# Optimization experiments

Hardware: AMD Instinct MI355X
Metric: run time of the kernel (lower is better)

Reference implementation:

```python
import jax, jax.numpy as jnp
import numpy as np

D_MODEL = 1024
N_HEADS = 16
N_GROUPS = 4
HEAD_DIM = D_MODEL // N_HEADS          # 64
HPG = N_HEADS // N_GROUPS              # heads per group = 4
KV_DIM = N_GROUPS * HEAD_DIM           # 256


def setup_inputs() -> dict:
    key = jax.random.key(0)
    ks = jax.random.split(key, 9)
    B, T = 2, 2048
    s = 0.02
    return {
        "x":  jax.random.normal(ks[0], (B, T, D_MODEL), dtype=jnp.float32),
        "Wq": jax.random.normal(ks[1], (D_MODEL, D_MODEL), dtype=jnp.float32) * s,
        "bq": jnp.zeros((D_MODEL,), dtype=jnp.float32),
        "Wk": jax.random.normal(ks[2], (D_MODEL, KV_DIM), dtype=jnp.float32) * s,
        "bk": jnp.zeros((KV_DIM,), dtype=jnp.float32),
        "Wv": jax.random.normal(ks[3], (D_MODEL, KV_DIM), dtype=jnp.float32) * s,
        "bv": jnp.zeros((KV_DIM,), dtype=jnp.float32),
        "Wo": jax.random.normal(ks[4], (D_MODEL, D_MODEL), dtype=jnp.float32) * s,
        "bo": jnp.zeros((D_MODEL,), dtype=jnp.float32),
    }


def reference(x, Wq, bq, Wk, bk, Wv, bv, Wo, bo):
    B, T, C = x.shape
    q = x @ Wq + bq                                   # [B,T,C]
    k = x @ Wk + bk                                   # [B,T,G*hd]
    v = x @ Wv + bv

    # [B, G, hpg, T, hd] for q; [B, G, T, hd] for k,v (native GQA head sharing,
    # equivalent to repeat_interleave on the group dim in the torch code)
    q = q.reshape(B, T, N_GROUPS, HPG, HEAD_DIM).transpose(0, 2, 3, 1, 4)
    k = k.reshape(B, T, N_GROUPS, HEAD_DIM).transpose(0, 2, 1, 3)
    v = v.reshape(B, T, N_GROUPS, HEAD_DIM).transpose(0, 2, 1, 3)

    scale = 1.0 / jnp.sqrt(jnp.float32(HEAD_DIM))
    attn = jnp.einsum('bghqd,bgkd->bghqk', q, k) * scale   # [B,G,hpg,T,T]

    causal = jnp.tril(jnp.ones((T, T), dtype=bool))        # True = keep
    attn = jnp.where(causal, attn, jnp.float32(-jnp.inf))
    attn = jax.nn.softmax(attn, axis=-1)
    # dropout p=0.1 only in training mode; reference is eval mode (identity)

    out = jnp.einsum('bghqk,bgkd->bghqd', attn, v)         # [B,G,hpg,T,hd]
    out = out.transpose(0, 3, 1, 2, 4).reshape(B, T, C)
    return out @ Wo + bo
```

## Files before the change

### kernel.cpp

```cpp
#include <hip/hip_runtime.h>
#include <hip/hip_bf16.h>
#include <stdint.h>

#define D_MODEL 1024
#define T_LEN   2048
#define BATCH   2
#define N_HEADS 16
#define KV_DIM  256
#define QKV_N   1536
#define M_ROWS  (BATCH * T_LEN)

typedef unsigned short u16;
typedef __bf16 bf16x8 __attribute__((ext_vector_type(8)));
typedef __bf16 bf16x2 __attribute__((ext_vector_type(2)));
typedef float  f32x4  __attribute__((ext_vector_type(4)));

__device__ __forceinline__ u16 f2b(float f) {
    uint32_t u = __builtin_bit_cast(uint32_t, f);
    u += 0x7FFFu + ((u >> 16) & 1u);
    return (u16)(u >> 16);
}

__device__ __forceinline__ uint32_t pk_bf16(float a, float b) {
#if __has_builtin(__builtin_amdgcn_cvt_pk_bf16_f32)
    bf16x2 v = __builtin_amdgcn_cvt_pk_bf16_f32(a, b);
    return __builtin_bit_cast(uint32_t, v);
#else
    return (uint32_t)f2b(a) | ((uint32_t)f2b(b) << 16);
#endif
}

__device__ __forceinline__ void gl_lds16(const void* g, void* l) {
    __builtin_amdgcn_global_load_lds(g, l, 16, 0, 0);
}

__global__ __launch_bounds__(256) void prep(
    const float* __restrict__ x,
    const float* __restrict__ Wq, const float* __restrict__ Wk,
    const float* __restrict__ Wv, const float* __restrict__ Wo,
    u16* __restrict__ xb, u16* __restrict__ WcatT, u16* __restrict__ WoT)
{
    __shared__ u16 tile[32][33];
    int id = blockIdx.x;
    int tid = threadIdx.x;
    if (id < 2048) {
        int i = (id * 256 + tid) * 8;
        float4 a = *(const float4*)&x[i];
        float4 c = *(const float4*)&x[i + 4];
        u16 r[8] = { f2b(a.x), f2b(a.y), f2b(a.z), f2b(a.w),
                     f2b(c.x), f2b(c.y), f2b(c.z), f2b(c.w) };
        *(uint4*)&xb[i] = *(const uint4*)r;
        return;
    }
    int t = id - 2048;
    int bx = t % 80;
    int k0 = (t / 80) * 32;
    const float* src; u16* dst; int N, n0;
    if (bx < 32)       { src = Wq; dst = WcatT;                   N = 1024; n0 = bx * 32; }
    else if (bx < 40)  { src = Wk; dst = WcatT + 1024 * 1024;     N = 256;  n0 = (bx - 32) * 32; }
    else if (bx < 48)  { src = Wv; dst = WcatT + 1280 * 1024;     N = 256;  n0 = (bx - 40) * 32; }
    else               { src = Wo; dst = WoT;                     N = 1024; n0 = (bx - 48) * 32; }
    for (int i = 0; i < 4; ++i) {
        int idx = tid + i * 256;
        int r = idx >> 5, c = idx & 31;
        tile[r][c] = f2b(src[(size_t)(k0 + r) * N + (n0 + c)]);
    }
    __syncthreads();
    for (int i = 0; i < 4; ++i) {
        int idx = tid + i * 256;
        int r = idx >> 5, c = idx & 31;
        dst[(size_t)(n0 + r) * 1024 + (k0 + c)] = tile[c][r];
    }
}

__global__ __launch_bounds__(256) void gemm_qkv(
    const u16* __restrict__ A, const u16* __restrict__ BT,
    const float* __restrict__ bq, const float* __restrict__ bk,
    const float* __restrict__ bv, u16* __restrict__ Qb,
    u16* __restrict__ Kpack, u16* __restrict__ Vpack)
{
    constexpr int K = 1024;
    constexpr float SCALE = 0.125f * 1.44269504088896f;
    __shared__ __align__(16) u16 As[64 * 64];
    __shared__ __align__(16) u16 Bs[128 * 64];

    int tid  = threadIdx.x;
    int lane = tid & 63, w = tid >> 6;
    int quad = lane >> 4, l15 = lane & 15;
    int m0 = blockIdx.y * 64, n0 = blockIdx.x * 128;
    int lr = lane >> 3, lc = (lane & 7) * 8;

    f32x4 acc[4][2] = {};

    for (int k0 = 0; k0 < K; k0 += 64) {
        for (int t = 0; t < 2; ++t) {
            int rb = t * 32 + w * 8;
            gl_lds16(&A[(size_t)(m0 + rb + lr) * K + k0 + lc], &As[rb * 64]);
        }
        for (int t = 0; t < 4; ++t) {
            int rb = t * 32 + w * 8;
            gl_lds16(&BT[(size_t)(n0 + rb + lr) * K + k0 + lc], &Bs[rb * 64]);
        }
        __syncthreads();
        for (int kk = 0; kk < 64; kk += 32) {
            bf16x8 a[4], b[2];
            for (int i = 0; i < 4; ++i)
                a[i] = *(const bf16x8*)&As[(i * 16 + l15) * 64 + kk + quad * 8];
            for (int j = 0; j < 2; ++j)
                b[j] = *(const bf16x8*)&Bs[(w * 32 + j * 16 + l15) * 64 + kk + quad * 8];
            for (int i = 0; i < 4; ++i)
                for (int j = 0; j < 2; ++j)
                    acc[i][j] = __builtin_amdgcn_mfma_f32_16x16x32_bf16(
                        a[i], b[j], acc[i][j], 0, 0, 0);
        }
        __syncthreads();
    }

    for (int j = 0; j < 2; ++j) {
        int col = n0 + w * 32 + j * 16 + l15;
        float bj = (col < 1024) ? bq[col] : (col < 1280) ? bk[col - 1024] : bv[col - 1280];
        for (int i = 0; i < 4; ++i) {
            int rowb = m0 + i * 16 + quad * 4;
            int bb = rowb >> 11, keyloc = rowb & 2047;
            int t64 = keyloc >> 6;
            if (col < 1024) {
                for (int r = 0; r < 4; ++r)
                    Qb[(size_t)(rowb + r) * 1024 + col] =
                        f2b((acc[i][j][r] + bj) * SCALE);
            } else if (col < 1280) {
                int d = col - 1024; int g = d >> 6; d &= 63;
                int kk = d >> 5, qd = (d >> 3) & 3, e = d & 7;
                int ntk = (keyloc >> 4) & 3, l15k = keyloc & 15;
                size_t base = ((((size_t)(bb * 4 + g) * 32 + t64) * 2 + kk) * 4
                               + ntk) * 512 + qd * 128 + l15k * 8 + e;
                for (int r = 0; r < 4; ++r)
                    Kpack[base + r * 8] = f2b(acc[i][j][r] + bj);
            } else {
                int d = col - 1280; int g = d >> 6; d &= 63;
                int dt = d >> 4, l15v = d & 15;
                int kkp = (keyloc >> 5) & 1, qv = (keyloc >> 3) & 3, e0 = keyloc & 7;
                u16 tmp[4];
                for (int r = 0; r < 4; ++r) tmp[r] = f2b(acc[i][j][r] + bj);
                size_t base = ((((size_t)(bb * 4 + g) * 32 + t64) * 2 + kkp) * 4
                               + dt) * 512 + (qv * 16 + l15v) * 8 + e0;
                *(uint64_t*)&Vpack[base] = *(const uint64_t*)tmp;
            }
        }
    }
}

__global__ __launch_bounds__(256) void gemm_out(
    const u16* __restrict__ A, const u16* __restrict__ BT,
    const float* __restrict__ bias, float* __restrict__ C)
{
    constexpr int K = 1024, N = 1024;
    __shared__ __align__(16) u16 As[64 * 64];
    __shared__ __align__(16) u16 Bs[128 * 64];

    int tid  = threadIdx.x;
    int lane = tid & 63, w = tid >> 6;
    int quad = lane >> 4, l15 = lane & 15;
    int m0 = blockIdx.y * 64, n0 = blockIdx.x * 128;
    int lr = lane >> 3, lc = (lane & 7) * 8;

    f32x4 acc[4][2] = {};

    for (int k0 = 0; k0 < K; k0 += 64) {
        for (int t = 0; t < 2; ++t) {
            int rb = t * 32 + w * 8;
            gl_lds16(&A[(size_t)(m0 + rb + lr) * K + k0 + lc], &As[rb * 64]);
        }
        for (int t = 0; t < 4; ++t) {
            int rb = t * 32 + w * 8;
            gl_lds16(&BT[(size_t)(n0 + rb + lr) * K + k0 + lc], &Bs[rb * 64]);
        }
        __syncthreads();
        for (int kk = 0; kk < 64; kk += 32) {
            bf16x8 a[4], b[2];
            for (int i = 0; i < 4; ++i)
                a[i] = *(const bf16x8*)&As[(i * 16 + l15) * 64 + kk + quad * 8];
            for (int j = 0; j < 2; ++j)
                b[j] = *(const bf16x8*)&Bs[(w * 32 + j * 16 + l15) * 64 + kk + quad * 8];
            for (int i = 0; i < 4; ++i)
                for (int j = 0; j < 2; ++j)
                    acc[i][j] = __builtin_amdgcn_mfma_f32_16x16x32_bf16(
                        a[i], b[j], acc[i][j], 0, 0, 0);
        }
        __syncthreads();
    }

    for (int j = 0; j < 2; ++j) {
        int col = n0 + w * 32 + j * 16 + l15;
        float bj = bias[col];
        for (int i = 0; i < 4; ++i) {
            int rowb = m0 + i * 16 + quad * 4;
            for (int r = 0; r < 4; ++r)
                C[(size_t)(rowb + r) * N + col] = acc[i][j][r] + bj;
        }
    }
}

__global__ __launch_bounds__(64, 4) void attn_kernel(
    const u16* __restrict__ Qb,
    const u16* __restrict__ Kpack,
    const u16* __restrict__ Vpack,
    u16* __restrict__ AO)
{
    constexpr int LDP = 72;
    __shared__ __align__(16) u16 Pw[16 * LDP];

    int lane = threadIdx.x & 63;
    int quad = lane >> 4, l15 = lane & 15;

    int gid = blockIdx.x;
    int b = gid & 1, g = (gid >> 1) & 3;
    int hw = (gid >> 3) & 3;
    int s = gid >> 5;
    int j = 127 - s;
    int head = g * 4 + hw;
    int q0 = j * 16;
    int iters = (j >> 2) + 1;

    const u16* Qp = Qb + ((size_t)b * T_LEN + q0) * 1024 + head * 64;
    const u16* Kp = Kpack + (size_t)(b * 4 + g) * 131072 + (size_t)lane * 8;
    const u16* Vp = Vpack + (size_t)(b * 4 + g) * 131072 + (size_t)lane * 8;
    u16*       Op = AO + ((size_t)b * T_LEN + q0) * D_MODEL + head * 64;

    bf16x8 Qfrag[2];
    #pragma unroll
    for (int kk = 0; kk < 2; ++kk)
        Qfrag[kk] = *(const bf16x8*)&Qp[(size_t)l15 * 1024 + kk * 32 + quad * 8];

    f32x4 o[4] = {};
    float lsum = 0.f;

    for (int tg = 0; tg < iters; ++tg) {
        bool diag = (tg == iters - 1);

        const u16* kb = Kp + (size_t)tg * 4096;
        bf16x8 aK[2][4];
        #pragma unroll
        for (int kk = 0; kk < 2; ++kk)
            #pragma unroll
            for (int ntk = 0; ntk < 4; ++ntk)
                aK[kk][ntk] = *(const bf16x8*)(kb + (kk * 4 + ntk) * 512);

        f32x4 sacc[4] = {};
        #pragma unroll
        for (int kk = 0; kk < 2; ++kk) {
            bf16x8 bQ = Qfrag[kk];
            #pragma unroll
            for (int ntk = 0; ntk < 4; ++ntk)
                sacc[ntk] = __builtin_amdgcn_mfma_f32_16x16x32_bf16(
                    aK[kk][ntk], bQ, sacc[ntk], 0, 0, 0);
        }
        int qrow = q0 + l15;
        float lacc = 0.f;
        #pragma unroll
        for (int ntk = 0; ntk < 4; ++ntk) {
            float p0, p1, p2, p3;
            if (diag) {
                int key = tg * 64 + ntk * 16 + quad * 4;
                p0 = (key + 0 <= qrow) ? exp2f(sacc[ntk][0]) : 0.f;
                p1 = (key + 1 <= qrow) ? exp2f(sacc[ntk][1]) : 0.f;
                p2 = (key + 2 <= qrow) ? exp2f(sacc[ntk][2]) : 0.f;
                p3 = (key + 3 <= qrow) ? exp2f(sacc[ntk][3]) : 0.f;
            } else {
                p0 = exp2f(sacc[ntk][0]);
                p1 = exp2f(sacc[ntk][1]);
                p2 = exp2f(sacc[ntk][2]);
                p3 = exp2f(sacc[ntk][3]);
            }
            lacc += (p0 + p1) + (p2 + p3);
            uint2 pv;
            pv.x = pk_bf16(p0, p1);
            pv.y = pk_bf16(p2, p3);
            *(uint2*)&Pw[l15 * LDP + ntk * 16 + quad * 4] = pv;
        }
        lsum += lacc;

        const u16* vb = Vp + (size_t)tg * 4096;
        #pragma unroll
        for (int kkp = 0; kkp < 2; ++kkp) {
            bf16x8 bV[4];
            #pragma unroll
            for (int dt = 0; dt < 4; ++dt)
                bV[dt] = *(const bf16x8*)(vb + (kkp * 4 + dt) * 512);
            bf16x8 aP = *(const bf16x8*)&Pw[l15 * LDP + kkp * 32 + quad * 8];
            #pragma unroll
            for (int dt = 0; dt < 4; ++dt)
                o[dt] = __builtin_amdgcn_mfma_f32_16x16x32_bf16(
                    aP, bV[dt], o[dt], 0, 0, 0);
        }
    }

    float l = lsum;
    l += __shfl_xor(l, 16, 64);
    l += __shfl_xor(l, 32, 64);
    float linv = 1.0f / l;
    float li[4];
    #pragma unroll
    for (int r = 0; r < 4; ++r)
        li[r] = __shfl(linv, quad * 4 + r, 64);
    #pragma unroll
    for (int dt = 0; dt < 4; ++dt)
        #pragma unroll
        for (int r = 0; r < 4; ++r)
            Op[(size_t)(quad * 4 + r) * D_MODEL + dt * 16 + l15] =
                f2b(o[dt][r] * li[r]);
}

extern "C" void kernel_launch(void* const* d_in, const int* in_sizes, int n_in,
                              void* d_out, int out_size, void* d_ws, size_t ws_size,
                              hipStream_t stream) {
    const float* x  = (const float*)d_in[0];
    const float* Wq = (const float*)d_in[1];
    const float* bq = (const float*)d_in[2];
    const float* Wk = (const float*)d_in[3];
    const float* bk = (const float*)d_in[4];
    const float* Wv = (const float*)d_in[5];
    const float* bv = (const float*)d_in[6];
    const float* Wo = (const float*)d_in[7];
    const float* bo = (const float*)d_in[8];
    float* out = (float*)d_out;

    u16* ws    = (u16*)d_ws;
    u16* xb    = ws;  ws += (size_t)M_ROWS * 1024;
    u16* WcatT = ws;  ws += (size_t)QKV_N * 1024;
    u16* WoT   = ws;  ws += 1024 * 1024;
    u16* Qb    = ws;  ws += (size_t)M_ROWS * 1024;
    u16* Kpack = ws;  ws += (size_t)M_ROWS * KV_DIM;
    u16* Vpack = ws;  ws += (size_t)M_ROWS * KV_DIM;
    u16* AO    = xb;

    prep<<<2048 + 2560, 256, 0, stream>>>(x, Wq, Wk, Wv, Wo, xb, WcatT, WoT);
    gemm_qkv<<<dim3(QKV_N / 128, M_ROWS / 64), 256, 0, stream>>>(
        xb, WcatT, bq, bk, bv, Qb, Kpack, Vpack);
    attn_kernel<<<4096, 64, 0, stream>>>(Qb, Kpack, Vpack, AO);
    gemm_out<<<dim3(1024 / 128, M_ROWS / 64), 256, 0, stream>>>(AO, WoT, bo, out);
}
```

Before: 188.3 us.

## Share K/V tiles across the four GQA heads via LDS in attention

The attention kernel now launches 256-thread blocks in which four wavefronts handle the four query heads of one KV group. Each K/V tile is loaded once into shared memory with direct global-to-LDS loads and reused by all four heads, which cuts redundant global K/V traffic by four. Query tiles are reordered so blocks with long and short causal workloads interleave, for load balance. The cost is two block-wide barriers per key tile and more LDS per block, and the load of each tile is not overlapped with compute.

New measurement: 177.8 us. -5.6%, faster.

```diff
diff --git a/kernel.cpp b/kernel.cpp
--- a/kernel.cpp
+++ b/kernel.cpp
@@ -200,31 +200,36 @@
     }
 }
 
-__global__ __launch_bounds__(64, 4) void attn_kernel(
+__global__ __launch_bounds__(256, 4) void attn_kernel(
     const u16* __restrict__ Qb,
     const u16* __restrict__ Kpack,
     const u16* __restrict__ Vpack,
     u16* __restrict__ AO)
 {
     constexpr int LDP = 72;
-    __shared__ __align__(16) u16 Pw[16 * LDP];
-
-    int lane = threadIdx.x & 63;
+    __shared__ __align__(16) u16 Kv[4096];
+    __shared__ __align__(16) u16 Vv[4096];
+    __shared__ __align__(16) u16 Ps[4][16 * LDP];
+
+    int tid  = threadIdx.x;
+    int lane = tid & 63, w = tid >> 6;
     int quad = lane >> 4, l15 = lane & 15;
 
     int gid = blockIdx.x;
     int b = gid & 1, g = (gid >> 1) & 3;
-    int hw = (gid >> 3) & 3;
-    int s = gid >> 5;
-    int j = 127 - s;
-    int head = g * 4 + hw;
+    int s = gid >> 3;
+    int kq = s >> 5, tq = s & 31;
+    int q4 = (kq & 1) ? tq : (31 - tq);
+    int j  = q4 * 4 + kq;
+    int head = g * 4 + w;
     int q0 = j * 16;
-    int iters = (j >> 2) + 1;
+    int iters = q4 + 1;
 
     const u16* Qp = Qb + ((size_t)b * T_LEN + q0) * 1024 + head * 64;
-    const u16* Kp = Kpack + (size_t)(b * 4 + g) * 131072 + (size_t)lane * 8;
-    const u16* Vp = Vpack + (size_t)(b * 4 + g) * 131072 + (size_t)lane * 8;
+    const u16* Kp = Kpack + (size_t)(b * 4 + g) * 131072;
+    const u16* Vp = Vpack + (size_t)(b * 4 + g) * 131072;
     u16*       Op = AO + ((size_t)b * T_LEN + q0) * D_MODEL + head * 64;
+    u16* Pw = Ps[w];
 
     bf16x8 Qfrag[2];
     #pragma unroll
@@ -237,22 +242,26 @@
     for (int tg = 0; tg < iters; ++tg) {
         bool diag = (tg == iters - 1);
 
-        const u16* kb = Kp + (size_t)tg * 4096;
-        bf16x8 aK[2][4];
-        #pragma unroll
-        for (int kk = 0; kk < 2; ++kk)
-            #pragma unroll
-            for (int ntk = 0; ntk < 4; ++ntk)
-                aK[kk][ntk] = *(const bf16x8*)(kb + (kk * 4 + ntk) * 512);
+        const u16* kt = Kp + (size_t)tg * 4096;
+        const u16* vt = Vp + (size_t)tg * 4096;
+        #pragma unroll
+        for (int c = 0; c < 2; ++c) {
+            int ch = w * 2 + c;
+            gl_lds16(kt + ch * 512 + lane * 8, &Kv[ch * 512]);
+            gl_lds16(vt + ch * 512 + lane * 8, &Vv[ch * 512]);
+        }
+        __syncthreads();
 
         f32x4 sacc[4] = {};
         #pragma unroll
         for (int kk = 0; kk < 2; ++kk) {
             bf16x8 bQ = Qfrag[kk];
             #pragma unroll
-            for (int ntk = 0; ntk < 4; ++ntk)
+            for (int ntk = 0; ntk < 4; ++ntk) {
+                bf16x8 aK = *(const bf16x8*)&Kv[(kk * 4 + ntk) * 512 + lane * 8];
                 sacc[ntk] = __builtin_amdgcn_mfma_f32_16x16x32_bf16(
-                    aK[kk][ntk], bQ, sacc[ntk], 0, 0, 0);
+                    aK, bQ, sacc[ntk], 0, 0, 0);
+            }
         }
         int qrow = q0 + l15;
         float lacc = 0.f;
@@ -279,19 +288,17 @@
         }
         lsum += lacc;
 
-        const u16* vb = Vp + (size_t)tg * 4096;
         #pragma unroll
         for (int kkp = 0; kkp < 2; ++kkp) {
-            bf16x8 bV[4];
-            #pragma unroll
-            for (int dt = 0; dt < 4; ++dt)
-                bV[dt] = *(const bf16x8*)(vb + (kkp * 4 + dt) * 512);
             bf16x8 aP = *(const bf16x8*)&Pw[l15 * LDP + kkp * 32 + quad * 8];
             #pragma unroll
-            for (int dt = 0; dt < 4; ++dt)
+            for (int dt = 0; dt < 4; ++dt) {
+                bf16x8 bV = *(const bf16x8*)&Vv[(kkp * 4 + dt) * 512 + lane * 8];
                 o[dt] = __builtin_amdgcn_mfma_f32_16x16x32_bf16(
-                    aP, bV[dt], o[dt], 0, 0, 0);
-        }
+                    aP, bV, o[dt], 0, 0, 0);
+            }
+        }
+        __syncthreads();
     }
 
     float l = lsum;
@@ -336,6 +343,6 @@
     prep<<<2048 + 2560, 256, 0, stream>>>(x, Wq, Wk, Wv, Wo, xb, WcatT, WoT);
     gemm_qkv<<<dim3(QKV_N / 128, M_ROWS / 64), 256, 0, stream>>>(
         xb, WcatT, bq, bk, bv, Qb, Kpack, Vpack);
-    attn_kernel<<<4096, 64, 0, stream>>>(Qb, Kpack, Vpack, AO);
+    attn_kernel<<<1024, 256, 0, stream>>>(Qb, Kpack, Vpack, AO);
     gemm_out<<<dim3(1024 / 128, M_ROWS / 64), 256, 0, stream>>>(AO, WoT, bo, out);
 }
```
